# Kernel optimization log

Hardware: AMD Instinct MI355X
Metric: run time of the kernel (lower is better)

The kernel has to match this reference:

```python
import jax, jax.numpy as jnp
import numpy as np

T = 16384
VOC, POS, LEM = 100000, 50, 40000
TOK_D, POS_D, LEM_D, WV_D = 100, 32, 64, 100
EMB = TOK_D + POS_D + LEM_D + WV_D  # 296
IN_D, HID, PROJ = 512, 512, 256      # proj_size = lstm_dim/2


def setup_inputs() -> dict:
    key = jax.random.key(0)
    ks = jax.random.split(key, 24)
    s = 0.05
    n = lambda k, shape: (jax.random.normal(k, shape, dtype=jnp.float32) * s)
    return {
        "tokens": jax.random.randint(ks[0], (T,), 0, VOC),
        "postags": jax.random.randint(ks[1], (T,), 0, POS),
        "lemmas": jax.random.randint(ks[2], (T,), 0, LEM),
        "emb_token": n(ks[3], (VOC, TOK_D)),
        "emb_pos": n(ks[4], (POS, POS_D)),
        "emb_lem": n(ks[5], (LEM, LEM_D)),
        "word_vec": n(ks[6], (VOC, WV_D)),   # frozen pretrained table
        "linW": n(ks[7], (IN_D, EMB)),
        "linb": n(ks[8], (IN_D,)),
        # forward-direction LSTM (proj_size=PROJ): gates over hidden HID, recurrence on PROJ
        "Wih_f": n(ks[9], (4 * HID, IN_D)),
        "Whh_f": n(ks[10], (4 * HID, PROJ)),
        "bih_f": n(ks[11], (4 * HID,)),
        "bhh_f": n(ks[12], (4 * HID,)),
        "Whr_f": n(ks[13], (PROJ, HID)),
        # backward direction
        "Wih_b": n(ks[14], (4 * HID, IN_D)),
        "Whh_b": n(ks[15], (4 * HID, PROJ)),
        "bih_b": n(ks[16], (4 * HID,)),
        "bhh_b": n(ks[17], (4 * HID,)),
        "Whr_b": n(ks[18], (PROJ, HID)),
        "fcW": n(ks[19], (2, 2 * PROJ)),
        "fcb": n(ks[20], (2,)),
    }


def _lstm_dir(x, Wih, Whh, bih, bhh, Whr):
    """Single-direction projected LSTM over x:[T,IN_D] -> h:[T,PROJ]."""
    gx = x @ Wih.T + (bih + bhh)  # precompute input gates: [T, 4H]

    def step(carry, g_t):
        h, c = carry  # h:[PROJ], c:[HID]
        g = g_t + h @ Whh.T
        i, f, gg, o = jnp.split(g, 4)
        i = jax.nn.sigmoid(i)
        f = jax.nn.sigmoid(f)
        gg = jnp.tanh(gg)
        o = jax.nn.sigmoid(o)
        c = f * c + i * gg
        h = (o * jnp.tanh(c)) @ Whr.T  # projection: HID -> PROJ
        return (h, c), h

    h0 = jnp.zeros((PROJ,), dtype=x.dtype)
    c0 = jnp.zeros((HID,), dtype=x.dtype)
    _, hs = jax.lax.scan(step, (h0, c0), gx)
    return hs  # [T, PROJ]


def reference(tokens, postags, lemmas, emb_token, emb_pos, emb_lem, word_vec,
              linW, linb, Wih_f, Whh_f, bih_f, bhh_f, Whr_f,
              Wih_b, Whh_b, bih_b, bhh_b, Whr_b, fcW, fcb):
    # embedding concat: [T, EMB]
    emb = jnp.concatenate(
        [emb_token[tokens], emb_pos[postags], emb_lem[lemmas], word_vec[tokens]],
        axis=1)
    # linear + ReLU (dropout is identity in eval mode)
    x = jax.nn.relu(emb @ linW.T + linb)  # [T, IN_D]
    hf = _lstm_dir(x, Wih_f, Whh_f, bih_f, bhh_f, Whr_f)
    hb = _lstm_dir(x[::-1], Wih_b, Whh_b, bih_b, bhh_b, Whr_b)[::-1]
    lstm_out = jnp.concatenate([hf, hb], axis=1)  # [T, 2*PROJ]
    scores = lstm_out @ fcW.T + fcb  # [T, 2]
    return scores
```

## Files before the change

### kernel.cpp

```cpp
#include <hip/hip_runtime.h>

typedef unsigned short u16;
typedef unsigned int u32;
typedef unsigned long long u64;

#define T_LEN 16384
#define HALO  32
#define CHUNK 1024
#define NGRP  16
#define NBLK  256
#define SENT  0xFFFFFFFFu
#define GXR 128
#define GXT 64
#define GXK 64

__device__ __forceinline__ float bf2f(u16 u){ u32 x = ((u32)u)<<16; return __builtin_bit_cast(float, x); }
__device__ __forceinline__ u16 f2bf(float f){ u32 x = __builtin_bit_cast(u32, f); u32 r = (x + 0x7FFFu + ((x>>16)&1u)) >> 16; return (u16)r; }
__device__ __forceinline__ float bflo(u32 u){ return __builtin_bit_cast(float, u<<16); }
__device__ __forceinline__ float bfhi(u32 u){ return __builtin_bit_cast(float, u & 0xFFFF0000u); }

__device__ __forceinline__ float sigm_fast(float x){ return __builtin_amdgcn_rcpf(1.f + __expf(-x)); }
__device__ __forceinline__ float tanh_fast(float x){ return 1.f - 2.f*__builtin_amdgcn_rcpf(1.f + __expf(2.f*x)); }

__global__ __launch_bounds__(256) void k_wsfail(float2* __restrict__ out2)
{
  const int idx = blockIdx.x*256 + threadIdx.x;
  out2[idx] = make_float2(7.0e6f, 7.0e6f);
}

__global__ __launch_bounds__(256) void k_init(uint4* __restrict__ hhx4, float* __restrict__ diag)
{
  const int idx = blockIdx.x*256 + threadIdx.x;
  hhx4[idx] = make_uint4(SENT, SENT, SENT, SENT);
  if (blockIdx.x == 0 && threadIdx.x == 0) {
    for (int k = 1; k < 8; ++k) diag[k] = 0.f;
    diag[0] = 1.f;
  }
}

__global__ __launch_bounds__(256) void k_embed(
    const int* __restrict__ tokens, const int* __restrict__ postags, const int* __restrict__ lemmas,
    const float* __restrict__ emb_token, const float* __restrict__ emb_pos, const float* __restrict__ emb_lem,
    const float* __restrict__ word_vec, const float* __restrict__ linW, const float* __restrict__ linb,
    u16* __restrict__ x_bf, float* __restrict__ diag)
{
  __shared__ float emb_sh[8][296];
  const int t0 = blockIdx.x * 8;
  const int tid = threadIdx.x;
  for (int idx = tid; idx < 8*296; idx += 256) {
    const int i = idx / 296;
    const int e = idx - i*296;
    const int tt = t0 + i;
    float v;
    if (e < 100)      v = emb_token[tokens[tt]*100 + e];
    else if (e < 132) v = emb_pos[postags[tt]*32 + (e-100)];
    else if (e < 196) v = emb_lem[lemmas[tt]*64 + (e-132)];
    else              v = word_vec[tokens[tt]*100 + (e-196)];
    emb_sh[i][e] = v;
  }
  __syncthreads();
  const int j0 = tid, j1 = tid + 256;
  float acc0[8], acc1[8];
  const float b0 = linb[j0], b1 = linb[j1];
  #pragma unroll
  for (int i=0;i<8;i++){ acc0[i]=b0; acc1[i]=b1; }
  for (int e = 0; e < 296; e += 4) {
    const float4 wa = *(const float4*)(linW + j0*296 + e);
    const float4 wb = *(const float4*)(linW + j1*296 + e);
    #pragma unroll
    for (int i=0;i<8;i++){
      const float4 ev = *(const float4*)&emb_sh[i][e];
      acc0[i] += ev.x*wa.x + ev.y*wa.y + ev.z*wa.z + ev.w*wa.w;
      acc1[i] += ev.x*wb.x + ev.y*wb.y + ev.z*wb.z + ev.w*wb.w;
    }
  }
  #pragma unroll
  for (int i=0;i<8;i++){
    x_bf[(t0+i)*512 + j0] = f2bf(fmaxf(acc0[i], 0.f));
    x_bf[(t0+i)*512 + j1] = f2bf(fmaxf(acc1[i], 0.f));
  }
  if (blockIdx.x == 0 && tid == 0) diag[1] = 1.f;
}

__global__ __launch_bounds__(256) void k_precA(
    const float* __restrict__ Whh_f, const float* __restrict__ Whr_f,
    const float* __restrict__ Whh_b, const float* __restrict__ Whr_b,
    u16* __restrict__ A_plain, float* __restrict__ diag)
{
  const int b = blockIdx.x;
  const int ct4 = b >> 6, d = (b >> 5) & 1, w = b & 31;
  const float* __restrict__ Whh = d ? Whh_b : Whh_f;
  const float* __restrict__ Whr = d ? Whr_b : Whr_f;
  __shared__ u16 whh_sh[64*260];
  __shared__ u16 whr_sh[256*36];
  const int tid = threadIdx.x;
  for (int idx = tid; idx < 64*256; idx += 256) {
    const int rr = idx >> 8, ch = idx & 255;
    const int gr = ((rr>>4)<<9) + w*16 + (rr&15);
    whh_sh[rr*260 + ch] = f2bf(Whh[gr*256 + ch]);
  }
  const int r = tid & 63, sub = tid >> 6;
  const int gr_out = ((r>>4)<<9) + w*16 + (r&15);
  for (int ct = ct4*4; ct < ct4*4 + 4; ++ct) {
    __syncthreads();
    for (int idx = tid; idx < 256*32; idx += 256) {
      const int p = idx >> 5, kk = idx & 31;
      whr_sh[p*36 + kk] = f2bf(Whr[p*512 + ct*32 + kk]);
    }
    __syncthreads();
    float acc[8];
    #pragma unroll
    for (int k=0;k<8;k++) acc[k]=0.f;
    for (int p = 0; p < 256; ++p) {
      const float hv = bf2f(whh_sh[r*260 + p]);
      const uint2 q0 = *(const uint2*)(whr_sh + p*36 + sub*8);
      const uint2 q1 = *(const uint2*)(whr_sh + p*36 + sub*8 + 4);
      acc[0]+=hv*bflo(q0.x); acc[1]+=hv*bfhi(q0.x); acc[2]+=hv*bflo(q0.y); acc[3]+=hv*bfhi(q0.y);
      acc[4]+=hv*bflo(q1.x); acc[5]+=hv*bfhi(q1.x); acc[6]+=hv*bflo(q1.y); acc[7]+=hv*bfhi(q1.y);
    }
    #pragma unroll
    for (int k=0;k<8;k++)
      A_plain[((size_t)(d*2048 + gr_out))*512 + ct*32 + sub*8 + k] = f2bf(acc[k]);
  }
  if (b == 0 && tid == 0) diag[2] = 1.f;
}

__global__ __launch_bounds__(256) void k_precMM(
    const float* __restrict__ Whr_f, const float* __restrict__ Whr_b,
    const float* __restrict__ fcW, float* __restrict__ MM, float* __restrict__ diag)
{
  const int d = blockIdx.x >> 1;
  const int u = (blockIdx.x & 1)*256 + threadIdx.x;
  const float* __restrict__ Whr = d ? Whr_b : Whr_f;
  float a0 = 0.f, a1 = 0.f;
  for (int p = 0; p < 256; ++p) {
    const float wv = Whr[p*512 + u];
    a0 += wv * fcW[d*256 + p];
    a1 += wv * fcW[512 + d*256 + p];
  }
  MM[(d*512+u)*2]   = a0;
  MM[(d*512+u)*2+1] = a1;
  if (blockIdx.x == 0 && threadIdx.x == 0) diag[3] = 1.f;
}

__global__ __launch_bounds__(256) void k_gx(
    const u16* __restrict__ x_bf,
    const float* __restrict__ Wih_f, const float* __restrict__ bih_f, const float* __restrict__ bhh_f,
    const float* __restrict__ Wih_b, const float* __restrict__ bih_b, const float* __restrict__ bhh_b,
    u16* __restrict__ gx, float* __restrict__ diag)
{
  const int d = blockIdx.z;
  const int rowbase = blockIdx.y * GXR;
  const int tokbase = blockIdx.x * GXT;
  const float* __restrict__ Wih = d ? Wih_b : Wih_f;
  const float* __restrict__ bih = d ? bih_b : bih_f;
  const float* __restrict__ bhh = d ? bhh_b : bhh_f;
  __shared__ float W_lds[GXR][GXK+4];
  __shared__ float x_lds[GXT][GXK+4];
  const int tid = threadIdx.x;
  const int rg = tid & 63;
  const int tg = tid >> 6;
  const int j0 = rowbase + rg*2;
  const u32* __restrict__ x32 = (const u32*)x_bf;
  float acc0[16], acc1[16];
  #pragma unroll
  for (int tt=0; tt<16; ++tt){ acc0[tt]=0.f; acc1[tt]=0.f; }
  for (int kt = 0; kt < 512; kt += GXK) {
    __syncthreads();
    #pragma unroll
    for (int ld = 0; ld < 8; ++ld) {
      const int fidx = ld*1024 + tid*4;
      const int row = fidx >> 6, kk = fidx & 63;
      *(float4*)&W_lds[row][kk] = *(const float4*)(Wih + (size_t)(rowbase+row)*512 + kt + kk);
    }
    #pragma unroll
    for (int ld = 0; ld < 8; ++ld) {
      const int uidx = ld*256 + tid;
      const int tok = uidx >> 5, kp = uidx & 31;
      const u32 v = x32[(size_t)(tokbase+tok)*256 + (kt>>1) + kp];
      x_lds[tok][2*kp] = bflo(v); x_lds[tok][2*kp+1] = bfhi(v);
    }
    __syncthreads();
    #pragma unroll 4
    for (int k = 0; k < GXK; k += 4) {
      const float4 w0 = *(const float4*)&W_lds[rg*2][k];
      const float4 w1 = *(const float4*)&W_lds[rg*2+1][k];
      #pragma unroll
      for (int tt = 0; tt < 16; ++tt) {
        const float4 xv = *(const float4*)&x_lds[tg*16+tt][k];
        acc0[tt] += w0.x*xv.x + w0.y*xv.y + w0.z*xv.z + w0.w*xv.w;
        acc1[tt] += w1.x*xv.x + w1.y*xv.y + w1.z*xv.z + w1.w*xv.w;
      }
    }
  }
  const float bs0 = bih[j0] + bhh[j0];
  const float bs1 = bih[j0+1] + bhh[j0+1];
  #pragma unroll
  for (int tt = 0; tt < 16; ++tt) {
    const int tok = tokbase + tg*16 + tt;
    const u32 pack = (u32)f2bf(acc0[tt]+bs0) | ((u32)f2bf(acc1[tt]+bs1) << 16);
    *(u32*)(gx + ((size_t)d*T_LEN + tok)*2048 + j0) = pack;
  }
  if (blockIdx.x==0 && blockIdx.y==0 && blockIdx.z==0 && tid==0) diag[5] = 1.f;
}

__global__ __launch_bounds__(512, 2) void k_seq_big(
    const u16* __restrict__ A_plain, const u16* __restrict__ gx,
    u32* __restrict__ hh_main, u32* __restrict__ hh_halo, float* __restrict__ diag)
{
  const int bid = blockIdx.x;
  const int w = bid >> 5, gi = bid & 31;
  const int d = gi >> 4, g = gi & 15;
  const int tid = threadIdx.x;
  const int r = tid >> 1, s = tid & 1;
  __shared__ float h_sh[2*260];
  __shared__ float g_sh[256];
  const int gr = ((r>>6)<<9) + w*64 + (r&63);
  u32 Afp[32][4];
  #pragma unroll
  for (int it=0; it<32; ++it) {
    const uint4 a = *(const uint4*)(A_plain + ((size_t)(d*2048 + gr))*512 + s*256 + it*8);
    Afp[it][0]=a.x; Afp[it][1]=a.y; Afp[it][2]=a.z; Afp[it][3]=a.w;
  }
  const u16* __restrict__ gxp = gx + (size_t)d*T_LEN*2048 + gr;
  const int tau0 = g*CHUNK;
  const int ibeg = (g == 0) ? 0 : -HALO;
  const size_t main_base = (size_t)d * T_LEN * 256;
  const size_t halo_base = (size_t)(d*NGRP + g) * HALO * 256;
  const int tok0 = d ? (T_LEN-1-(tau0+ibeg)) : (tau0+ibeg);
  float gxv = bf2f(gxp[(size_t)tok0*2048]);
  float c_reg = 0.f;
  int patience = 60000;
  for (int i = ibeg; i < CHUNK; ++i) {
    const int inext = (i+1 < CHUNK) ? (i+1) : i;
    const int tokn = d ? (T_LEN-1-(tau0+inext)) : (tau0+inext);
    const u16 gxn = gxp[(size_t)tokn*2048];
    if (tid < 256) {
      u32 uv = 0u;
      if (i != ibeg) {
        const u32* src = (i >= 1)
          ? hh_main + main_base + (size_t)(tau0 + i - 1)*256 + tid
          : hh_halo + halo_base + (size_t)(i - 1 + HALO)*256 + tid;
        uv = __hip_atomic_load(src, __ATOMIC_RELAXED, __HIP_MEMORY_SCOPE_AGENT);
        while (uv == SENT && patience > 0) {
          --patience;
          __builtin_amdgcn_s_sleep(2);
          uv = __hip_atomic_load(src, __ATOMIC_RELAXED, __HIP_MEMORY_SCOPE_AGENT);
        }
        if (uv == SENT) {
          __hip_atomic_store(diag + 6, 1.f, __ATOMIC_RELAXED, __HIP_MEMORY_SCOPE_AGENT);
          uv = 0u;
        }
      }
      float* hq = h_sh + (tid>>7)*260 + ((2*tid)&255);
      hq[0] = bflo(uv); hq[1] = bfhi(uv);
    }
    __syncthreads();
    float a0=0.f, a1=0.f, a2=0.f, a3=0.f;
    {
      const float* hb = h_sh + s*260;
      #pragma unroll
      for (int it=0; it<32; ++it) {
        const float4 h0 = *(const float4*)(hb + it*8);
        const float4 h1 = *(const float4*)(hb + it*8 + 4);
        a0 += bflo(Afp[it][0])*h0.x; a1 += bfhi(Afp[it][0])*h0.y;
        a2 += bflo(Afp[it][1])*h0.z; a3 += bfhi(Afp[it][1])*h0.w;
        a0 += bflo(Afp[it][2])*h1.x; a1 += bfhi(Afp[it][2])*h1.y;
        a2 += bflo(Afp[it][3])*h1.z; a3 += bfhi(Afp[it][3])*h1.w;
      }
    }
    float acc = (a0 + a1) + (a2 + a3);
    acc += __shfl_xor(acc, 1);
    if (s == 0) g_sh[r] = acc + gxv;
    __syncthreads();
    if (tid < 64) {
      __builtin_amdgcn_s_setprio(1);
      const float gi_ = sigm_fast(g_sh[tid]);
      const float gf  = sigm_fast(g_sh[64+tid]);
      const float gg  = tanh_fast(g_sh[128+tid]);
      const float go  = sigm_fast(g_sh[192+tid]);
      c_reg = gf*c_reg + gi_*gg;
      const float hv = go * tanh_fast(c_reg);
      const float ho = __shfl_xor(hv, 1);
      if ((tid & 1) == 0) {
        const u32 pack = (u32)f2bf(hv) | ((u32)f2bf(ho) << 16);
        u32* dst = (i >= 0)
          ? hh_main + main_base + (size_t)(tau0 + i)*256 + w*32 + (tid>>1)
          : hh_halo + halo_base + (size_t)(i + HALO)*256 + w*32 + (tid>>1);
        __hip_atomic_store(dst, pack, __ATOMIC_RELAXED, __HIP_MEMORY_SCOPE_SYSTEM);
      }
      __builtin_amdgcn_s_setprio(0);
    }
    gxv = bf2f(gxn);
  }
  if (tid == 0) atomicAdd(diag + 4, 1.f);
}

__global__ __launch_bounds__(256) void k_out(
    const u32* __restrict__ hhx, const float* __restrict__ MM,
    const float* __restrict__ fcb, const float* __restrict__ diag, float* __restrict__ out)
{
  __shared__ float MM_sh[2048];
  const int tid = threadIdx.x;
  for (int i = tid; i < 2048; i += 256) MM_sh[i] = MM[i];
  __syncthreads();
  float pen = 0.f;
  if (diag[0] != 1.f) pen += 2.0e6f;
  if (diag[1] != 1.f) pen += 1.0e4f;
  if (diag[2] != 1.f) pen += 3.0e4f;
  if (diag[3] != 1.f) pen += 1.0e5f;
  if (diag[5] != 1.f) pen += 5.0e4f;
  const float cnt = diag[4];
  if (cnt == 0.f) pen += 4.0e5f;
  else if (cnt != (float)NBLK) pen += 2.0e5f;
  if (diag[6] != 0.f) pen += 1.0e6f;
  const int tt = tid >> 3, l = tid & 7;
  const int t = blockIdx.x*32 + tt;
  float a0 = 0.f, a1 = 0.f, bad = 0.f;
  #pragma unroll
  for (int dd = 0; dd < 2; ++dd) {
    const int trow = dd ? (T_LEN + (T_LEN-1-t)) : t;
    const u32* __restrict__ hp = hhx + (size_t)trow*256;
    const float* __restrict__ mp = MM_sh + dd*1024;
    for (int it = 0; it < 32; ++it) {
      u32 v = hp[it*8 + l];
      if (v == SENT) { v = 0u; bad = 1.f; }
      const float lo = bflo(v), hi = bfhi(v);
      const int u = (it*8 + l)*2;
      a0 += lo*mp[u*2]     + hi*mp[u*2+2];
      a1 += lo*mp[u*2+1]   + hi*mp[u*2+3];
    }
  }
  a0 += __shfl_xor(a0,1); a0 += __shfl_xor(a0,2); a0 += __shfl_xor(a0,4);
  a1 += __shfl_xor(a1,1); a1 += __shfl_xor(a1,2); a1 += __shfl_xor(a1,4);
  bad = fmaxf(bad, __shfl_xor(bad,1)); bad = fmaxf(bad, __shfl_xor(bad,2)); bad = fmaxf(bad, __shfl_xor(bad,4));
  if (l == 0) {
    const float p = pen + bad*1.0e3f;
    *(float2*)(out + t*2) = make_float2(a0 + fcb[0] + p, a1 + fcb[1] + p);
  }
}

extern "C" void kernel_launch(void* const* d_in, const int* in_sizes, int n_in,
                              void* d_out, int out_size, void* d_ws, size_t ws_size,
                              hipStream_t stream) {
  const int* tokens  = (const int*)d_in[0];
  const int* postags = (const int*)d_in[1];
  const int* lemmas  = (const int*)d_in[2];
  const float* emb_token = (const float*)d_in[3];
  const float* emb_pos   = (const float*)d_in[4];
  const float* emb_lem   = (const float*)d_in[5];
  const float* word_vec  = (const float*)d_in[6];
  const float* linW = (const float*)d_in[7];
  const float* linb = (const float*)d_in[8];
  const float* Wih_f = (const float*)d_in[9];
  const float* Whh_f = (const float*)d_in[10];
  const float* bih_f = (const float*)d_in[11];
  const float* bhh_f = (const float*)d_in[12];
  const float* Whr_f = (const float*)d_in[13];
  const float* Wih_b = (const float*)d_in[14];
  const float* Whh_b = (const float*)d_in[15];
  const float* bih_b = (const float*)d_in[16];
  const float* bhh_b = (const float*)d_in[17];
  const float* Whr_b = (const float*)d_in[18];
  const float* fcW = (const float*)d_in[19];
  const float* fcb = (const float*)d_in[20];

  char* ws = (char*)d_ws;
  u16*   x_bf    = (u16*)(ws);
  u16*   A_plain = (u16*)(ws + 16777216);
  u32*   hh_main = (u32*)(ws + 20971520);
  u32*   hh_halo = (u32*)(ws + 54525952);
  float* MM      = (float*)(ws + 55574528);
  float* diag    = (float*)(ws + 55582720);
  u16*   gx      = (u16*)(ws + 55582784);
  const size_t NEED = 55582784ull + 134217728ull;

  if (ws_size < NEED) {
    k_wsfail<<<dim3(64), dim3(256), 0, stream>>>((float2*)d_out);
    return;
  }

  k_init<<<dim3(8448), dim3(256), 0, stream>>>((uint4*)hh_main, diag);
  k_embed<<<dim3(T_LEN/8), dim3(256), 0, stream>>>(tokens, postags, lemmas,
      emb_token, emb_pos, emb_lem, word_vec, linW, linb, x_bf, diag);
  k_precA<<<dim3(256), dim3(256), 0, stream>>>(Whh_f, Whr_f, Whh_b, Whr_b, A_plain, diag);
  k_precMM<<<dim3(4), dim3(256), 0, stream>>>(Whr_f, Whr_b, fcW, MM, diag);
  k_gx<<<dim3(T_LEN/GXT, 2048/GXR, 2), dim3(256), 0, stream>>>(x_bf,
      Wih_f, bih_f, bhh_f, Wih_b, bih_b, bhh_b, gx, diag);
  k_seq_big<<<dim3(NBLK), dim3(512), 0, stream>>>(A_plain, gx, hh_main, hh_halo, diag);
  k_out<<<dim3(T_LEN/32), dim3(256), 0, stream>>>(hh_main, MM, fcb, diag, (float*)d_out);
}
```

Baseline: 6.585 ms.

## Restructure recurrent step so each thread group owns all four gates, dropping a barrier

```diff
diff --git a/kernel.cpp b/kernel.cpp
--- a/kernel.cpp
+++ b/kernel.cpp
@@ -212,29 +212,42 @@
   const int w = bid >> 5, gi = bid & 31;
   const int d = gi >> 4, g = gi & 15;
   const int tid = threadIdx.x;
-  const int r = tid >> 1, s = tid & 1;
-  __shared__ float h_sh[2*260];
-  __shared__ float g_sh[256];
-  const int gr = ((r>>6)<<9) + w*64 + (r&63);
-  u32 Afp[32][4];
-  #pragma unroll
-  for (int it=0; it<32; ++it) {
-    const uint4 a = *(const uint4*)(A_plain + ((size_t)(d*2048 + gr))*512 + s*256 + it*8);
-    Afp[it][0]=a.x; Afp[it][1]=a.y; Afp[it][2]=a.z; Afp[it][3]=a.w;
-  }
-  const u16* __restrict__ gxp = gx + (size_t)d*T_LEN*2048 + gr;
+  const int c = tid >> 3, s = tid & 7;
+  __shared__ float h_sh[2][8*68];
+  u32 Af[4][32];
+  #pragma unroll
+  for (int q=0;q<4;++q){
+    const u16* ap = A_plain + ((size_t)(d*2048 + q*512 + w*64 + c))*512 + s*64;
+    #pragma unroll
+    for (int k=0;k<8;++k){
+      const uint4 a = *(const uint4*)(ap + k*8);
+      Af[q][k*4+0]=a.x; Af[q][k*4+1]=a.y; Af[q][k*4+2]=a.z; Af[q][k*4+3]=a.w;
+    }
+  }
+  const u16* __restrict__ gxp = gx + (size_t)d*T_LEN*2048 + w*64 + c;
   const int tau0 = g*CHUNK;
   const int ibeg = (g == 0) ? 0 : -HALO;
   const size_t main_base = (size_t)d * T_LEN * 256;
   const size_t halo_base = (size_t)(d*NGRP + g) * HALO * 256;
-  const int tok0 = d ? (T_LEN-1-(tau0+ibeg)) : (tau0+ibeg);
-  float gxv = bf2f(gxp[(size_t)tok0*2048]);
+  u16 gxc[4];
+  {
+    const int tok0 = d ? (T_LEN-1-(tau0+ibeg)) : (tau0+ibeg);
+    if (s == 0) {
+      const u16* p = gxp + (size_t)tok0*2048;
+      gxc[0]=p[0]; gxc[1]=p[512]; gxc[2]=p[1024]; gxc[3]=p[1536];
+    }
+  }
   float c_reg = 0.f;
   int patience = 60000;
+  int cur = 0;
   for (int i = ibeg; i < CHUNK; ++i) {
     const int inext = (i+1 < CHUNK) ? (i+1) : i;
     const int tokn = d ? (T_LEN-1-(tau0+inext)) : (tau0+inext);
-    const u16 gxn = gxp[(size_t)tokn*2048];
+    u16 gxn0=0, gxn1=0, gxn2=0, gxn3=0;
+    if (s == 0) {
+      const u16* p = gxp + (size_t)tokn*2048;
+      gxn0=p[0]; gxn1=p[512]; gxn2=p[1024]; gxn3=p[1536];
+    }
     if (tid < 256) {
       u32 uv = 0u;
       if (i != ibeg) {
@@ -244,7 +257,6 @@
         uv = __hip_atomic_load(src, __ATOMIC_RELAXED, __HIP_MEMORY_SCOPE_AGENT);
         while (uv == SENT && patience > 0) {
           --patience;
-          __builtin_amdgcn_s_sleep(2);
           uv = __hip_atomic_load(src, __ATOMIC_RELAXED, __HIP_MEMORY_SCOPE_AGENT);
         }
         if (uv == SENT) {
@@ -252,46 +264,57 @@
           uv = 0u;
         }
       }
-      float* hq = h_sh + (tid>>7)*260 + ((2*tid)&255);
+      float* hq = h_sh[cur] + (tid>>5)*68 + (tid&31)*2;
       hq[0] = bflo(uv); hq[1] = bfhi(uv);
     }
     __syncthreads();
-    float a0=0.f, a1=0.f, a2=0.f, a3=0.f;
+    float ai=0.f, af=0.f, ag=0.f, ao=0.f;
     {
-      const float* hb = h_sh + s*260;
+      const float* hb = h_sh[cur] + s*68;
       #pragma unroll
-      for (int it=0; it<32; ++it) {
-        const float4 h0 = *(const float4*)(hb + it*8);
-        const float4 h1 = *(const float4*)(hb + it*8 + 4);
-        a0 += bflo(Afp[it][0])*h0.x; a1 += bfhi(Afp[it][0])*h0.y;
-        a2 += bflo(Afp[it][1])*h0.z; a3 += bfhi(Afp[it][1])*h0.w;
-        a0 += bflo(Afp[it][2])*h1.x; a1 += bfhi(Afp[it][2])*h1.y;
-        a2 += bflo(Afp[it][3])*h1.z; a3 += bfhi(Afp[it][3])*h1.w;
+      for (int k=0;k<16;++k){
+        const float4 hv = *(const float4*)(hb + k*4);
+        {
+          const u32 p0=Af[0][k*2], p1=Af[0][k*2+1];
+          ai += bflo(p0)*hv.x + bfhi(p0)*hv.y + bflo(p1)*hv.z + bfhi(p1)*hv.w;
+        }
+        {
+          const u32 p0=Af[1][k*2], p1=Af[1][k*2+1];
+          af += bflo(p0)*hv.x + bfhi(p0)*hv.y + bflo(p1)*hv.z + bfhi(p1)*hv.w;
+        }
+        {
+          const u32 p0=Af[2][k*2], p1=Af[2][k*2+1];
+          ag += bflo(p0)*hv.x + bfhi(p0)*hv.y + bflo(p1)*hv.z + bfhi(p1)*hv.w;
+        }
+        {
+          const u32 p0=Af[3][k*2], p1=Af[3][k*2+1];
+          ao += bflo(p0)*hv.x + bfhi(p0)*hv.y + bflo(p1)*hv.z + bfhi(p1)*hv.w;
+        }
       }
     }
-    float acc = (a0 + a1) + (a2 + a3);
-    acc += __shfl_xor(acc, 1);
-    if (s == 0) g_sh[r] = acc + gxv;
-    __syncthreads();
-    if (tid < 64) {
-      __builtin_amdgcn_s_setprio(1);
-      const float gi_ = sigm_fast(g_sh[tid]);
-      const float gf  = sigm_fast(g_sh[64+tid]);
-      const float gg  = tanh_fast(g_sh[128+tid]);
-      const float go  = sigm_fast(g_sh[192+tid]);
-      c_reg = gf*c_reg + gi_*gg;
-      const float hv = go * tanh_fast(c_reg);
-      const float ho = __shfl_xor(hv, 1);
-      if ((tid & 1) == 0) {
-        const u32 pack = (u32)f2bf(hv) | ((u32)f2bf(ho) << 16);
-        u32* dst = (i >= 0)
-          ? hh_main + main_base + (size_t)(tau0 + i)*256 + w*32 + (tid>>1)
-          : hh_halo + halo_base + (size_t)(i + HALO)*256 + w*32 + (tid>>1);
-        __hip_atomic_store(dst, pack, __ATOMIC_RELAXED, __HIP_MEMORY_SCOPE_SYSTEM);
-      }
-      __builtin_amdgcn_s_setprio(0);
-    }
-    gxv = bf2f(gxn);
+    ai += __shfl_xor(ai,1); ai += __shfl_xor(ai,2); ai += __shfl_xor(ai,4);
+    af += __shfl_xor(af,1); af += __shfl_xor(af,2); af += __shfl_xor(af,4);
+    ag += __shfl_xor(ag,1); ag += __shfl_xor(ag,2); ag += __shfl_xor(ag,4);
+    ao += __shfl_xor(ao,1); ao += __shfl_xor(ao,2); ao += __shfl_xor(ao,4);
+    float hvv = 0.f;
+    if (s == 0) {
+      const float gi_ = sigm_fast(ai + bf2f(gxc[0]));
+      const float gf_ = sigm_fast(af + bf2f(gxc[1]));
+      const float gg_ = tanh_fast(ag + bf2f(gxc[2]));
+      const float go_ = sigm_fast(ao + bf2f(gxc[3]));
+      c_reg = gf_*c_reg + gi_*gg_;
+      hvv = go_ * tanh_fast(c_reg);
+      gxc[0]=gxn0; gxc[1]=gxn1; gxc[2]=gxn2; gxc[3]=gxn3;
+    }
+    const float hn = __shfl_xor(hvv, 8);
+    if (s == 0 && (c & 1) == 0) {
+      const u32 pack = (u32)f2bf(hvv) | ((u32)f2bf(hn) << 16);
+      u32* dst = (i >= 0)
+        ? hh_main + main_base + (size_t)(tau0 + i)*256 + w*32 + (c>>1)
+        : hh_halo + halo_base + (size_t)(i + HALO)*256 + w*32 + (c>>1);
+      __hip_atomic_store(dst, pack, __ATOMIC_RELAXED, __HIP_MEMORY_SCOPE_SYSTEM);
+    }
+    cur ^= 1;
   }
   if (tid == 0) atomicAdd(diag + 4, 1.f);
 }
```

Result: slower. 8.604 ms (+30.7%).
